# Kernel tuning notes

Measured on AMD Instinct MI355X. Metric: run time of the kernel, lower is better.

The kernel has to match this reference:

```python
import jax, jax.numpy as jnp
import numpy as np

DIM, HEADS, FFN, E = 1024, 16, 4096, 8
B, S = 2, 1024
EPS = 1e-5


def _ln(x, g, b):
    mu = jnp.mean(x, axis=-1, keepdims=True)
    var = jnp.mean((x - mu) ** 2, axis=-1, keepdims=True)
    return (x - mu) * jax.lax.rsqrt(var + EPS) * g + b


def setup_inputs() -> dict:
    key = jax.random.key(0)
    ks = jax.random.split(key, 20)
    sd = 0.02
    d, f = DIM, FFN
    return {
        "x": jax.random.normal(ks[0], (B, S, d), jnp.float32),
        "ln1_g": jnp.ones((d,), jnp.float32), "ln1_b": jnp.zeros((d,), jnp.float32),
        "Wqkv": jax.random.normal(ks[1], (d, 3 * d), jnp.float32) * sd,
        "bqkv": jnp.zeros((3 * d,), jnp.float32),
        "Wo": jax.random.normal(ks[2], (d, d), jnp.float32) * sd,
        "bo": jnp.zeros((d,), jnp.float32),
        "ln2_g": jnp.ones((d,), jnp.float32), "ln2_b": jnp.zeros((d,), jnp.float32),
        "gate_w": jax.random.normal(ks[3], (d, E), jnp.float32) * sd,
        "W1": jax.random.normal(ks[4], (E, d, f), jnp.float32) * sd,
        "b1": jnp.zeros((E, f), jnp.float32),
        "W2": jax.random.normal(ks[5], (E, f, d), jnp.float32) * sd,
        "b2": jnp.zeros((E, d), jnp.float32),
        "rW1": jax.random.normal(ks[6], (d, f), jnp.float32) * sd,
        "rb1": jnp.zeros((f,), jnp.float32),
        "rW2": jax.random.normal(ks[7], (f, d), jnp.float32) * sd,
        "rb2": jnp.zeros((d,), jnp.float32),
        "coef_w": jax.random.normal(ks[8], (d, 2), jnp.float32) * sd,
        "coef_b": jnp.zeros((2,), jnp.float32),
    }


def reference(x, ln1_g, ln1_b, Wqkv, bqkv, Wo, bo, ln2_g, ln2_b, gate_w,
              W1, b1, W2, b2, rW1, rb1, rW2, rb2, coef_w, coef_b):
    b, s, d = x.shape
    h, dh = HEADS, d // HEADS

    # --- attention block ---
    xn = _ln(x, ln1_g, ln1_b)
    qkv = xn @ Wqkv + bqkv                       # [b,s,3d]
    q, k, v = jnp.split(qkv, 3, axis=-1)
    q = q.reshape(b, s, h, dh)
    k = k.reshape(b, s, h, dh)
    v = v.reshape(b, s, h, dh)
    scores = jnp.einsum("bqhd,bkhd->bhqk", q, k) / jnp.sqrt(jnp.float32(dh))
    attn = jax.nn.softmax(scores, axis=-1)
    ctx = jnp.einsum("bhqk,bkhd->bqhd", attn, v).reshape(b, s, d)
    x = x + ctx @ Wo + bo

    # --- MoE FFN block (top-1 gating, DeepSpeed residual MoE) ---
    xn2 = _ln(x, ln2_g, ln2_b)
    xt = xn2.reshape(b * s, d)                   # [T,d] tokens
    probs = jax.nn.softmax(xt @ gate_w, axis=-1)  # [T,E]
    gate_val = jnp.max(probs, axis=-1, keepdims=True)   # top-1 prob
    expert_idx = jnp.argmax(probs, axis=-1)
    oh = jax.nn.one_hot(expert_idx, E, dtype=xt.dtype)  # [T,E] dispatch mask

    xe = jnp.einsum("te,td->etd", oh, xt)        # dispatch [E,T,d]
    he = jax.nn.gelu(jnp.einsum("etd,edf->etf", xe, W1) + b1[:, None, :], approximate=False)
    ye = jnp.einsum("etf,efd->etd", he, W2) + b2[:, None, :]
    moe_out = jnp.einsum("te,etd->td", oh, ye) * gate_val  # combine [T,d]

    # residual dense expert + learned mixing coefficient
    rm = jax.nn.gelu(xt @ rW1 + rb1, approximate=False) @ rW2 + rb2
    coef = jax.nn.softmax(xt @ coef_w + coef_b, axis=-1)  # [T,2]
    ff = moe_out * coef[:, 0:1] + rm * coef[:, 1:2]

    return x + ff.reshape(b, s, d)
```

## Files before the change

### kernel.cpp

```cpp
#include <hip/hip_runtime.h>
#include <math.h>

#define TOK 2048
#define NDIM 1024

typedef __attribute__((ext_vector_type(4))) float f32x4;
typedef __attribute__((ext_vector_type(8))) short s16x8;
typedef __attribute__((ext_vector_type(4))) short s16x4;

__device__ __forceinline__ short f2bf(float x) {
  unsigned int u = __builtin_bit_cast(unsigned int, x);
  unsigned int r = (u + 0x7fffu + ((u >> 16) & 1u)) >> 16;
  return (short)r;
}
__device__ __forceinline__ void gload_lds16(const void* g, void* l) {
  __builtin_amdgcn_global_load_lds((const __attribute__((address_space(1))) void*)g,
                                   (__attribute__((address_space(3))) void*)l, 16, 0, 0);
}

struct PackP { const float* src; short* dst; int K, N, nkt; };
__global__ __launch_bounds__(256)
void pack_k(PackP p)
{
  __shared__ float T[64 * 65];
  const int e = blockIdx.y;
  const int nkt = p.nkt;
  const int nt = blockIdx.x / nkt, kt = blockIdx.x % nkt;
  const float* src = p.src + (size_t)e * p.K * p.N + (size_t)(kt * 64) * p.N + nt * 64;
  const int t = threadIdx.x;
  #pragma unroll
  for (int i = 0; i < 16; ++i) {
    const int k = i * 4 + (t >> 6);
    T[k * 65 + (t & 63)] = src[(size_t)k * p.N + (t & 63)];
  }
  __syncthreads();
  short* dst = p.dst + ((size_t)e * gridDim.x + blockIdx.x) * 4096 + t * 16;
  s16x8 v[2];
  #pragma unroll
  for (int j2 = 0; j2 < 2; ++j2) {
    const int chunk = t * 2 + j2;
    const int col = chunk >> 3, od = chunk & 7, o = od ^ (col & 7);
    #pragma unroll
    for (int j = 0; j < 8; ++j) v[j2][j] = f2bf(T[(o * 8 + j) * 65 + col]);
  }
  *(s16x8*)dst = v[0];
  *(s16x8*)(dst + 8) = v[1];
}

__global__ __launch_bounds__(256)
void ln_k(const float* __restrict__ x, const float* __restrict__ g,
          const float* __restrict__ bb, short* __restrict__ out)
{
  const int row = blockIdx.x, tid = threadIdx.x;
  const f32x4 xv = *(const f32x4*)(x + (size_t)row * NDIM + tid * 4);
  float s = xv[0] + xv[1] + xv[2] + xv[3];
  float s2 = xv[0]*xv[0] + xv[1]*xv[1] + xv[2]*xv[2] + xv[3]*xv[3];
  #pragma unroll
  for (int m = 1; m < 64; m <<= 1) { s += __shfl_xor(s, m); s2 += __shfl_xor(s2, m); }
  __shared__ float red[8];
  const int w = tid >> 6, l = tid & 63;
  if (l == 0) { red[w] = s; red[4 + w] = s2; }
  __syncthreads();
  s = red[0] + red[1] + red[2] + red[3];
  s2 = red[4] + red[5] + red[6] + red[7];
  const float mean = s * (1.0f / NDIM);
  const float var = s2 * (1.0f / NDIM) - mean * mean;
  const float rstd = rsqrtf(var + 1e-5f);
  const f32x4 gv = *(const f32x4*)(g + tid * 4);
  const f32x4 bv = *(const f32x4*)(bb + tid * 4);
  s16x4 ov;
  #pragma unroll
  for (int j = 0; j < 4; ++j) ov[j] = f2bf((xv[j] - mean) * rstd * gv[j] + bv[j]);
  *(s16x4*)(out + (size_t)row * NDIM + tid * 4) = ov;
}

__global__ __launch_bounds__(256)
void gate_k(const float* __restrict__ x1, const float* __restrict__ g,
            const float* __restrict__ bb, const float* __restrict__ gw,
            const float* __restrict__ cw, const float* __restrict__ cb,
            int* __restrict__ counts, int* __restrict__ bucket,
            float* __restrict__ gs, float* __restrict__ c1o)
{
  const int tid = threadIdx.x, l = tid & 63, w = tid >> 6;
  const int t = blockIdx.x * 4 + w;
  f32x4 xv[4];
  #pragma unroll
  for (int it = 0; it < 4; ++it)
    xv[it] = *(const f32x4*)(x1 + (size_t)t * NDIM + it * 256 + l * 4);
  float s = 0.f, s2 = 0.f;
  #pragma unroll
  for (int it = 0; it < 4; ++it)
    #pragma unroll
    for (int j = 0; j < 4; ++j) { s += xv[it][j]; s2 += xv[it][j] * xv[it][j]; }
  #pragma unroll
  for (int m = 1; m < 64; m <<= 1) { s += __shfl_xor(s, m); s2 += __shfl_xor(s2, m); }
  const float mean = s * (1.0f / NDIM);
  const float rstd = rsqrtf(s2 * (1.0f / NDIM) - mean * mean + 1e-5f);
  float acc[10];
  #pragma unroll
  for (int j = 0; j < 10; ++j) acc[j] = 0.f;
  #pragma unroll
  for (int it = 0; it < 4; ++it) {
    #pragma unroll
    for (int j = 0; j < 4; ++j) {
      const int d0 = it * 256 + l * 4 + j;
      const float xn = (xv[it][j] - mean) * rstd * g[d0] + bb[d0];
      const f32x4 g0 = *(const f32x4*)(gw + (size_t)d0 * 8);
      const f32x4 g1 = *(const f32x4*)(gw + (size_t)d0 * 8 + 4);
      #pragma unroll
      for (int q = 0; q < 4; ++q) { acc[q] += xn * g0[q]; acc[4 + q] += xn * g1[q]; }
      acc[8] += xn * cw[d0 * 2]; acc[9] += xn * cw[d0 * 2 + 1];
    }
  }
  #pragma unroll
  for (int j = 0; j < 10; ++j)
    #pragma unroll
    for (int m = 1; m < 64; m <<= 1) acc[j] += __shfl_xor(acc[j], m);
  if (l == 0) {
    int best = 0; float mx = acc[0];
    #pragma unroll
    for (int e = 1; e < 8; ++e) if (acc[e] > mx) { mx = acc[e]; best = e; }
    float se = 0.f;
    #pragma unroll
    for (int e = 0; e < 8; ++e) se += __expf(acc[e] - mx);
    const float gate_val = 1.0f / se;
    const float l0 = acc[8] + cb[0], l1 = acc[9] + cb[1];
    const float cmx = fmaxf(l0, l1);
    const float e0 = __expf(l0 - cmx), e1 = __expf(l1 - cmx);
    const float inv = 1.0f / (e0 + e1);
    const int pos = atomicAdd(&counts[best], 1);
    bucket[best * TOK + pos] = t;
    gs[t] = gate_val * e0 * inv;
    c1o[t] = e1 * inv;
  }
}

struct GemmP {
  const short* A; const short* Bp; const float* bias;
  float* outf; short* outh;
  const float* resid; const float* aux; const float* sA; const float* sB;
  const int* bucket; const int* counts;
  int N, K, ktc;
};

template<int EPI, bool GATHER>
__global__ __launch_bounds__(256, 3)
void gemm_k(GemmP p)
{
  __shared__ short Al[2][8192];
  __shared__ short Bl[2][4096];
  const int tid = threadIdx.x;
  const int l = tid & 63, w = tid >> 6;
  const int wr = w >> 1, wc = w & 1;
  const int ntn = p.N >> 6, nkt = p.K >> 6;
  const int mt = blockIdx.x / ntn;
  const int nt = blockIdx.x % ntn;
  const int z = blockIdx.z;
  const bool first = (z == 0);
  const int K = p.K, N = p.N;

  int cnt = TOK;
  const short* Abase = p.A;
  const float* bias = p.bias;
  const int* bucket = nullptr;
  int e = 0;
  if (GATHER) {
    e = blockIdx.y;
    cnt = p.counts[e];
    if (mt * 128 >= cnt) return;
    bucket = p.bucket + e * TOK;
    bias = p.bias + (size_t)e * N;
  }
  const short* btile = p.Bp + ((size_t)(e * ntn + nt) * nkt) * 4096;

  const short* aptr[4];
  #pragma unroll
  for (int i = 0; i < 4; ++i) {
    const int rl = (i * 256 + tid) >> 3;
    int row;
    if (GATHER) {
      const int bidx = mt * 128 + rl;
      row = bucket[bidx < cnt ? bidx : mt * 128];
    } else row = mt * 128 + rl;
    aptr[i] = Abase + (size_t)row * K + ((tid & 7) ^ (rl & 7)) * 8;
  }

  const int kt0 = z * p.ktc, kt1 = kt0 + p.ktc;

  auto stage = [&](int kt, int buf) {
    const short* bsrc = btile + kt * 4096;
    #pragma unroll
    for (int j = 0; j < 2; ++j)
      gload_lds16(bsrc + (j * 256 + tid) * 8, (char*)Bl[buf] + (j * 256 + (tid & 192)) * 16);
    #pragma unroll
    for (int i = 0; i < 4; ++i)
      gload_lds16(aptr[i] + kt * 64, (char*)Al[buf] + (i * 256 + (tid & 192)) * 16);
  };

  f32x4 acc[4][2] = {};
  stage(kt0, 0);
  __syncthreads();
  for (int kt = kt0; kt < kt1; ++kt) {
    const int cur = (kt - kt0) & 1;
    if (kt + 1 < kt1) stage(kt + 1, cur ^ 1);
    #pragma unroll
    for (int ks = 0; ks < 2; ++ks) {
      const int octd = (ks * 4 + (l >> 4)) ^ (l & 7);
      s16x8 af[4], bfr[2];
      #pragma unroll
      for (int mf = 0; mf < 4; ++mf)
        af[mf] = *(const s16x8*)((char*)Al[cur] +
            (wr * 64 + mf * 16 + (l & 15)) * 128 + octd * 16);
      #pragma unroll
      for (int nf = 0; nf < 2; ++nf)
        bfr[nf] = *(const s16x8*)((char*)Bl[cur] +
            (wc * 32 + nf * 16 + (l & 15)) * 128 + octd * 16);
      #pragma unroll
      for (int mf = 0; mf < 4; ++mf)
        #pragma unroll
        for (int nf = 0; nf < 2; ++nf)
          acc[mf][nf] = __builtin_amdgcn_mfma_f32_16x16x32_bf16(af[mf], bfr[nf], acc[mf][nf], 0, 0, 0);
    }
    __syncthreads();
  }

  #pragma unroll
  for (int mf = 0; mf < 4; ++mf) {
    #pragma unroll
    for (int i = 0; i < 4; ++i) {
      const int rloc = wr * 64 + mf * 16 + (l >> 4) * 4 + i;
      int grow; bool valid = true;
      if (GATHER) {
        const int bidx = mt * 128 + rloc;
        valid = bidx < cnt;
        grow = valid ? bucket[bidx] : 0;
      } else grow = mt * 128 + rloc;
      float srow = 0.f;
      if (EPI == 3) srow = valid ? p.sA[grow] : 0.f;
      if (EPI == 4) srow = p.sB[grow];
      #pragma unroll
      for (int nf = 0; nf < 2; ++nf) {
        const int col = nt * 64 + wc * 32 + nf * 16 + (l & 15);
        const size_t off = (size_t)grow * N + col;
        const float bc = first ? bias[col] : 0.f;
        if (EPI == 0) {
          if (valid) p.outh[off] = f2bf(acc[mf][nf][i] + bc);
        } else if (EPI == 1) {
          const float v = acc[mf][nf][i] + bc;
          const float gv = 0.5f * v * (1.0f + erff(v * 0.70710678f));
          if (valid) p.outh[off] = f2bf(gv);
        } else if (EPI == 2) {
          atomicAdd(&p.outf[off], acc[mf][nf][i] + bc + (first ? p.resid[off] : 0.f));
        } else if (EPI == 3) {
          if (valid) atomicAdd(&p.outf[off], (acc[mf][nf][i] + bc) * srow);
        } else if (EPI == 4) {
          atomicAdd(&p.outf[off], (acc[mf][nf][i] + bc) * srow +
                    (first ? p.resid[off] + p.aux[off] : 0.f));
        }
      }
    }
  }
}

__global__ __launch_bounds__(256, 2)
void attn_k(const short* __restrict__ qkv, short* __restrict__ ctx)
{
  __shared__ short Klds[64 * 64];
  __shared__ short Vlds[64 * 64];
  __shared__ short Plds[4 * 16 * 64];
  const int tid = threadIdx.x, l = tid & 63, w = tid >> 6;
  const int qt = blockIdx.x;
  const int bh = blockIdx.y;
  const int b = bh >> 4, h = bh & 15;
  const size_t tbase = (size_t)b * 1024;

  const int sq = qt * 64 + w * 16 + (l & 15);
  s16x8 qf[2];
  #pragma unroll
  for (int ks = 0; ks < 2; ++ks)
    qf[ks] = *(const s16x8*)(qkv + (tbase + sq) * 3072 + h * 64 + ks * 32 + (l >> 4) * 8);

  f32x4 o[4] = {};
  float mrow[4], lrow[4];
  #pragma unroll
  for (int i = 0; i < 4; ++i) { mrow[i] = -1e30f; lrow[i] = 0.f; }

  for (int kt = 0; kt < 16; ++kt) {
    #pragma unroll
    for (int i = 0; i < 2; ++i) {
      const int s = i * 256 + tid;
      const int r = s >> 3, c = s & 7, csrc = c ^ (r & 7);
      const short* gsrc = qkv + (tbase + kt * 64 + r) * 3072 + 1024 + h * 64 + csrc * 8;
      gload_lds16(gsrc, (char*)Klds + (i * 256 + (tid & 192)) * 16);
    }
    #pragma unroll
    for (int i = 0; i < 2; ++i) {
      const int kv0 = (i * 4 + w) * 8;
      s16x8 vv;
      #pragma unroll
      for (int j = 0; j < 8; ++j)
        vv[j] = qkv[(tbase + kt * 64 + kv0 + j) * 3072 + 2048 + h * 64 + l];
      *(s16x8*)((char*)Vlds + ((l * 128 + kv0 * 2) ^ ((l & 7) << 4))) = vv;
    }
    __syncthreads();

    f32x4 sv[4];
    #pragma unroll
    for (int nf = 0; nf < 4; ++nf) {
      f32x4 a = {0.f, 0.f, 0.f, 0.f};
      const int kv = nf * 16 + (l & 15);
      #pragma unroll
      for (int ks = 0; ks < 2; ++ks) {
        const s16x8 kb = *(const s16x8*)((char*)Klds +
            ((kv * 128 + (ks * 32 + (l >> 4) * 8) * 2) ^ ((kv & 7) << 4)));
        a = __builtin_amdgcn_mfma_f32_16x16x32_bf16(qf[ks], kb, a, 0, 0, 0);
      }
      sv[nf] = a * 0.125f;
    }
    float sc[4], ps[4];
    #pragma unroll
    for (int i = 0; i < 4; ++i) {
      float m = fmaxf(fmaxf(sv[0][i], sv[1][i]), fmaxf(sv[2][i], sv[3][i]));
      #pragma unroll
      for (int msk = 1; msk < 16; msk <<= 1) m = fmaxf(m, __shfl_xor(m, msk));
      const float mn = fmaxf(mrow[i], m);
      sc[i] = __expf(mrow[i] - mn);
      mrow[i] = mn;
      ps[i] = 0.f;
    }
    #pragma unroll
    for (int nf = 0; nf < 4; ++nf)
      #pragma unroll
      for (int i = 0; i < 4; ++i) {
        const float pp = __expf(sv[nf][i] - mrow[i]);
        sv[nf][i] = pp;
        ps[i] += pp;
      }
    #pragma unroll
    for (int i = 0; i < 4; ++i) {
      #pragma unroll
      for (int msk = 1; msk < 16; msk <<= 1) ps[i] += __shfl_xor(ps[i], msk);
      lrow[i] = lrow[i] * sc[i] + ps[i];
    }
    #pragma unroll
    for (int nf = 0; nf < 4; ++nf)
      #pragma unroll
      for (int i = 0; i < 4; ++i) o[nf][i] *= sc[i];

    char* pw = (char*)Plds + w * 2048;
    #pragma unroll
    for (int nf = 0; nf < 4; ++nf)
      #pragma unroll
      for (int i = 0; i < 4; ++i) {
        const int q = (l >> 4) * 4 + i;
        *(short*)(pw + ((q * 128 + (nf * 16 + (l & 15)) * 2) ^ ((q & 7) << 4))) = f2bf(sv[nf][i]);
      }
    __syncthreads();
    #pragma unroll
    for (int ks = 0; ks < 2; ++ks) {
      const s16x8 pa = *(const s16x8*)(pw +
          (((l & 15) * 128 + (ks * 32 + (l >> 4) * 8) * 2) ^ ((l & 7) << 4)));
      #pragma unroll
      for (int nf = 0; nf < 4; ++nf) {
        const int dh = nf * 16 + (l & 15);
        const s16x8 vb = *(const s16x8*)((char*)Vlds +
            ((dh * 128 + (ks * 32 + (l >> 4) * 8) * 2) ^ ((dh & 7) << 4)));
        o[nf] = __builtin_amdgcn_mfma_f32_16x16x32_bf16(pa, vb, o[nf], 0, 0, 0);
      }
    }
    __syncthreads();
  }
  #pragma unroll
  for (int i = 0; i < 4; ++i) {
    const float inv = 1.0f / lrow[i];
    const size_t t = tbase + qt * 64 + w * 16 + (l >> 4) * 4 + i;
    #pragma unroll
    for (int nf = 0; nf < 4; ++nf)
      ctx[t * 1024 + h * 64 + nf * 16 + (l & 15)] = f2bf(o[nf][i] * inv);
  }
}

extern "C" void kernel_launch(void* const* d_in, const int* in_sizes, int n_in,
                              void* d_out, int out_size, void* d_ws, size_t ws_size,
                              hipStream_t stream)
{
  const float* x    = (const float*)d_in[0];
  const float* ln1g = (const float*)d_in[1];
  const float* ln1b = (const float*)d_in[2];
  const float* Wqkv = (const float*)d_in[3];
  const float* bqkv = (const float*)d_in[4];
  const float* Wo   = (const float*)d_in[5];
  const float* bo   = (const float*)d_in[6];
  const float* ln2g = (const float*)d_in[7];
  const float* ln2b = (const float*)d_in[8];
  const float* gw   = (const float*)d_in[9];
  const float* W1   = (const float*)d_in[10];
  const float* b1   = (const float*)d_in[11];
  const float* W2   = (const float*)d_in[12];
  const float* b2   = (const float*)d_in[13];
  const float* rW1  = (const float*)d_in[14];
  const float* rb1  = (const float*)d_in[15];
  const float* rW2  = (const float*)d_in[16];
  const float* rb2  = (const float*)d_in[17];
  const float* cw   = (const float*)d_in[18];
  const float* cb   = (const float*)d_in[19];
  float* out = (float*)d_out;

  char* ws = (char*)d_ws;
  const size_t MB = 1024 * 1024;
  short* xn1    = (short*)(ws + 0);
  short* qkv    = (short*)(ws + 4 * MB);
  short* he     = (short*)(ws + 4 * MB);
  short* ctx    = (short*)(ws + 16 * MB);
  float* x1     = (float*)(ws + 20 * MB);
  short* xn2    = (short*)(ws + 28 * MB);
  short* hr     = (short*)(ws + 32 * MB);
  float* moe    = (float*)(ws + 48 * MB);
  int*   counts = (int*)(ws + 56 * MB);
  int*   bucket = (int*)(ws + 56 * MB + 256);
  float* gs     = (float*)(ws + 56 * MB + 256 + 64 * 1024);
  float* c1     = (float*)(ws + 56 * MB + 256 + 64 * 1024 + 8192);
  short* Wqkvp  = (short*)(ws + 64 * MB);
  short* Wop    = (short*)(ws + 70 * MB);
  short* W1p    = (short*)(ws + 72 * MB);
  short* W2p    = (short*)(ws + 136 * MB);
  short* rW1p   = (short*)(ws + 200 * MB);
  short* rW2p   = (short*)(ws + 208 * MB);

  hipMemsetAsync(counts, 0, 8 * sizeof(int), stream);
  hipMemsetAsync(x1, 0, TOK * NDIM * sizeof(float), stream);
  hipMemsetAsync(moe, 0, TOK * NDIM * sizeof(float), stream);
  hipMemsetAsync(out, 0, TOK * NDIM * sizeof(float), stream);

  PackP pk;
  pk = PackP{Wqkv, Wqkvp, 1024, 3072, 16}; pack_k<<<dim3(48 * 16, 1), 256, 0, stream>>>(pk);
  pk = PackP{Wo,   Wop,   1024, 1024, 16}; pack_k<<<dim3(16 * 16, 1), 256, 0, stream>>>(pk);
  pk = PackP{W1,   W1p,   1024, 4096, 16}; pack_k<<<dim3(64 * 16, 8), 256, 0, stream>>>(pk);
  pk = PackP{W2,   W2p,   4096, 1024, 64}; pack_k<<<dim3(16 * 64, 8), 256, 0, stream>>>(pk);
  pk = PackP{rW1,  rW1p,  1024, 4096, 16}; pack_k<<<dim3(64 * 16, 1), 256, 0, stream>>>(pk);
  pk = PackP{rW2,  rW2p,  4096, 1024, 64}; pack_k<<<dim3(16 * 64, 1), 256, 0, stream>>>(pk);

  ln_k<<<TOK, 256, 0, stream>>>(x, ln1g, ln1b, xn1);

  GemmP p{};
  p.A = xn1; p.Bp = Wqkvp; p.bias = bqkv; p.outh = qkv; p.N = 3072; p.K = 1024; p.ktc = 16;
  gemm_k<0, false><<<dim3(16 * 48), 256, 0, stream>>>(p);

  attn_k<<<dim3(16, 32), 256, 0, stream>>>(qkv, ctx);

  p = GemmP{};
  p.A = ctx; p.Bp = Wop; p.bias = bo; p.outf = x1; p.resid = x; p.N = 1024; p.K = 1024; p.ktc = 8;
  gemm_k<2, false><<<dim3(16 * 16, 1, 2), 256, 0, stream>>>(p);

  ln_k<<<TOK, 256, 0, stream>>>(x1, ln2g, ln2b, xn2);
  gate_k<<<TOK / 4, 256, 0, stream>>>(x1, ln2g, ln2b, gw, cw, cb, counts, bucket, gs, c1);

  p = GemmP{};
  p.A = xn2; p.Bp = W1p; p.bias = b1; p.outh = he; p.N = 4096; p.K = 1024; p.ktc = 16;
  p.bucket = bucket; p.counts = counts;
  gemm_k<1, true><<<dim3(16 * 64, 8), 256, 0, stream>>>(p);

  p = GemmP{};
  p.A = he; p.Bp = W2p; p.bias = b2; p.outf = moe; p.sA = gs; p.N = 1024; p.K = 4096; p.ktc = 16;
  p.bucket = bucket; p.counts = counts;
  gemm_k<3, true><<<dim3(16 * 16, 8, 4), 256, 0, stream>>>(p);

  p = GemmP{};
  p.A = xn2; p.Bp = rW1p; p.bias = rb1; p.outh = hr; p.N = 4096; p.K = 1024; p.ktc = 16;
  gemm_k<1, false><<<dim3(16 * 64), 256, 0, stream>>>(p);

  p = GemmP{};
  p.A = hr; p.Bp = rW2p; p.bias = rb2; p.outf = out; p.resid = x1; p.aux = moe; p.sB = c1;
  p.N = 1024; p.K = 4096; p.ktc = 16;
  gemm_k<4, false><<<dim3(16 * 16, 1, 4), 256, 0, stream>>>(p);
}
```

Before: 511.3 us.

## Merge dense residual FFN into grouped MoE GEMMs and tighten GEMM pipeline sync

The residual dense FFN GEMMs become a ninth 'expert' slice of the grouped W1 and W2 launches. The second of these accumulates straight into the output, so the separate moe buffer, its memset and two launches go away. The GEMM main loop replaces __syncthreads with explicit vmcnt waits and raw s_barrier, so the next tile's loads can stay in flight while the current tile is computed. The weight pack kernel now reads float4 rows and handles four 64-column tiles per block, which cuts block count and makes the global reads coalesced. The risks are more atomic contention on the output and a hand-written vmcnt(6) that must match the number of issued loads exactly.

Result: faster. 488.2 us (-4.5%).

```diff
diff --git a/kernel.cpp b/kernel.cpp
--- a/kernel.cpp
+++ b/kernel.cpp
@@ -22,29 +22,37 @@
 __global__ __launch_bounds__(256)
 void pack_k(PackP p)
 {
-  __shared__ float T[64 * 65];
-  const int e = blockIdx.y;
+  __shared__ short T[64][264];
   const int nkt = p.nkt;
-  const int nt = blockIdx.x / nkt, kt = blockIdx.x % nkt;
-  const float* src = p.src + (size_t)e * p.K * p.N + (size_t)(kt * 64) * p.N + nt * 64;
+  const int cb = blockIdx.x / nkt, kt = blockIdx.x % nkt;
+  const int ntn = p.N >> 6;
+  const float* src = p.src + (size_t)blockIdx.y * p.K * p.N + (size_t)(kt * 64) * p.N + cb * 256;
   const int t = threadIdx.x;
   #pragma unroll
   for (int i = 0; i < 16; ++i) {
-    const int k = i * 4 + (t >> 6);
-    T[k * 65 + (t & 63)] = src[(size_t)k * p.N + (t & 63)];
+    const int r = i * 4 + (t >> 6);
+    const f32x4 v = *(const f32x4*)(src + (size_t)r * p.N + (t & 63) * 4);
+    short* d = &T[r][(t & 63) * 4];
+    d[0] = f2bf(v[0]); d[1] = f2bf(v[1]); d[2] = f2bf(v[2]); d[3] = f2bf(v[3]);
   }
   __syncthreads();
-  short* dst = p.dst + ((size_t)e * gridDim.x + blockIdx.x) * 4096 + t * 16;
-  s16x8 v[2];
-  #pragma unroll
-  for (int j2 = 0; j2 < 2; ++j2) {
-    const int chunk = t * 2 + j2;
-    const int col = chunk >> 3, od = chunk & 7, o = od ^ (col & 7);
-    #pragma unroll
-    for (int j = 0; j < 8; ++j) v[j2][j] = f2bf(T[(o * 8 + j) * 65 + col]);
-  }
-  *(s16x8*)dst = v[0];
-  *(s16x8*)(dst + 8) = v[1];
+  #pragma unroll
+  for (int j = 0; j < 4; ++j) {
+    short* dst = p.dst + ((size_t)(blockIdx.y * ntn + cb * 4 + j) * nkt + kt) * 4096 + t * 16;
+    s16x8 v0, v1;
+    #pragma unroll
+    for (int jj = 0; jj < 2; ++jj) {
+      const int chunk = t * 2 + jj;
+      const int col = chunk >> 3, od = chunk & 7, o = od ^ (col & 7);
+      #pragma unroll
+      for (int kk = 0; kk < 8; ++kk) {
+        const short vv = T[o * 8 + kk][j * 64 + col];
+        if (jj == 0) v0[kk] = vv; else v1[kk] = vv;
+      }
+    }
+    *(s16x8*)dst = v0;
+    *(s16x8*)(dst + 8) = v1;
+  }
 }
 
 __global__ __launch_bounds__(256)
@@ -136,14 +144,15 @@
 }
 
 struct GemmP {
-  const short* A; const short* Bp; const float* bias;
-  float* outf; short* outh;
-  const float* resid; const float* aux; const float* sA; const float* sB;
+  const short* A; const short* A2; const short* Bp; const short* Bp2;
+  const float* bias; const float* bias2;
+  short* outh; short* outh2; float* outf;
+  const float* resid; const float* gs; const float* c1;
   const int* bucket; const int* counts;
   int N, K, ktc;
 };
 
-template<int EPI, bool GATHER>
+template<int MODE>
 __global__ __launch_bounds__(256, 3)
 void gemm_k(GemmP p)
 {
@@ -159,26 +168,29 @@
   const bool first = (z == 0);
   const int K = p.K, N = p.N;
 
-  int cnt = TOK;
-  const short* Abase = p.A;
-  const float* bias = p.bias;
+  int e = 0, cnt = TOK;
   const int* bucket = nullptr;
-  int e = 0;
-  if (GATHER) {
+  if (MODE >= 2) {
     e = blockIdx.y;
-    cnt = p.counts[e];
-    if (mt * 128 >= cnt) return;
-    bucket = p.bucket + e * TOK;
-    bias = p.bias + (size_t)e * N;
-  }
-  const short* btile = p.Bp + ((size_t)(e * ntn + nt) * nkt) * 4096;
+    if (e < 8) {
+      cnt = p.counts[e];
+      if (mt * 128 >= cnt) return;
+      bucket = p.bucket + e * TOK;
+    }
+  }
+  const short* Abase = (MODE == 3 && e == 8) ? p.A2 : p.A;
+  const float* bias = (MODE >= 2) ? (e < 8 ? p.bias + (size_t)e * N : p.bias2) : p.bias;
+  const short* btile = (MODE >= 2)
+      ? (e < 8 ? p.Bp + ((size_t)(e * ntn + nt) * nkt) * 4096
+               : p.Bp2 + ((size_t)nt * nkt) * 4096)
+      : p.Bp + ((size_t)nt * nkt) * 4096;
 
   const short* aptr[4];
   #pragma unroll
   for (int i = 0; i < 4; ++i) {
     const int rl = (i * 256 + tid) >> 3;
     int row;
-    if (GATHER) {
+    if (bucket) {
       const int bidx = mt * 128 + rl;
       row = bucket[bidx < cnt ? bidx : mt * 128];
     } else row = mt * 128 + rl;
@@ -199,10 +211,15 @@
 
   f32x4 acc[4][2] = {};
   stage(kt0, 0);
-  __syncthreads();
   for (int kt = kt0; kt < kt1; ++kt) {
     const int cur = (kt - kt0) & 1;
-    if (kt + 1 < kt1) stage(kt + 1, cur ^ 1);
+    if (kt + 1 < kt1) {
+      stage(kt + 1, cur ^ 1);
+      asm volatile("s_waitcnt vmcnt(6)" ::: "memory");
+    } else {
+      asm volatile("s_waitcnt vmcnt(0)" ::: "memory");
+    }
+    __builtin_amdgcn_s_barrier();
     #pragma unroll
     for (int ks = 0; ks < 2; ++ks) {
       const int octd = (ks * 4 + (l >> 4)) ^ (l & 7);
@@ -221,41 +238,41 @@
         for (int nf = 0; nf < 2; ++nf)
           acc[mf][nf] = __builtin_amdgcn_mfma_f32_16x16x32_bf16(af[mf], bfr[nf], acc[mf][nf], 0, 0, 0);
     }
-    __syncthreads();
-  }
-
+    asm volatile("" ::: "memory");
+    __builtin_amdgcn_s_barrier();
+  }
+
+  short* oh = (MODE == 2) ? (e < 8 ? p.outh : p.outh2) : p.outh;
   #pragma unroll
   for (int mf = 0; mf < 4; ++mf) {
     #pragma unroll
     for (int i = 0; i < 4; ++i) {
       const int rloc = wr * 64 + mf * 16 + (l >> 4) * 4 + i;
       int grow; bool valid = true;
-      if (GATHER) {
+      if (bucket) {
         const int bidx = mt * 128 + rloc;
         valid = bidx < cnt;
         grow = valid ? bucket[bidx] : 0;
       } else grow = mt * 128 + rloc;
-      float srow = 0.f;
-      if (EPI == 3) srow = valid ? p.sA[grow] : 0.f;
-      if (EPI == 4) srow = p.sB[grow];
+      float srow = 1.f;
+      if (MODE == 3) srow = (e < 8) ? (valid ? p.gs[grow] : 0.f) : p.c1[grow];
       #pragma unroll
       for (int nf = 0; nf < 2; ++nf) {
         const int col = nt * 64 + wc * 32 + nf * 16 + (l & 15);
         const size_t off = (size_t)grow * N + col;
         const float bc = first ? bias[col] : 0.f;
-        if (EPI == 0) {
-          if (valid) p.outh[off] = f2bf(acc[mf][nf][i] + bc);
-        } else if (EPI == 1) {
+        if (MODE == 0) {
+          oh[off] = f2bf(acc[mf][nf][i] + bc);
+        } else if (MODE == 1) {
+          atomicAdd(&p.outf[off], acc[mf][nf][i] + bc + (first ? p.resid[off] : 0.f));
+        } else if (MODE == 2) {
           const float v = acc[mf][nf][i] + bc;
           const float gv = 0.5f * v * (1.0f + erff(v * 0.70710678f));
-          if (valid) p.outh[off] = f2bf(gv);
-        } else if (EPI == 2) {
-          atomicAdd(&p.outf[off], acc[mf][nf][i] + bc + (first ? p.resid[off] : 0.f));
-        } else if (EPI == 3) {
-          if (valid) atomicAdd(&p.outf[off], (acc[mf][nf][i] + bc) * srow);
-        } else if (EPI == 4) {
-          atomicAdd(&p.outf[off], (acc[mf][nf][i] + bc) * srow +
-                    (first ? p.resid[off] + p.aux[off] : 0.f));
+          if (valid) oh[off] = f2bf(gv);
+        } else if (MODE == 3) {
+          if (valid)
+            atomicAdd(&p.outf[off], (acc[mf][nf][i] + bc) * srow +
+                      ((e == 8 && first) ? p.resid[off] : 0.f));
         }
       }
     }
@@ -415,7 +432,6 @@
   float* x1     = (float*)(ws + 20 * MB);
   short* xn2    = (short*)(ws + 28 * MB);
   short* hr     = (short*)(ws + 32 * MB);
-  float* moe    = (float*)(ws + 48 * MB);
   int*   counts = (int*)(ws + 56 * MB);
   int*   bucket = (int*)(ws + 56 * MB + 256);
   float* gs     = (float*)(ws + 56 * MB + 256 + 64 * 1024);
@@ -429,48 +445,40 @@
 
   hipMemsetAsync(counts, 0, 8 * sizeof(int), stream);
   hipMemsetAsync(x1, 0, TOK * NDIM * sizeof(float), stream);
-  hipMemsetAsync(moe, 0, TOK * NDIM * sizeof(float), stream);
   hipMemsetAsync(out, 0, TOK * NDIM * sizeof(float), stream);
 
   PackP pk;
-  pk = PackP{Wqkv, Wqkvp, 1024, 3072, 16}; pack_k<<<dim3(48 * 16, 1), 256, 0, stream>>>(pk);
-  pk = PackP{Wo,   Wop,   1024, 1024, 16}; pack_k<<<dim3(16 * 16, 1), 256, 0, stream>>>(pk);
-  pk = PackP{W1,   W1p,   1024, 4096, 16}; pack_k<<<dim3(64 * 16, 8), 256, 0, stream>>>(pk);
-  pk = PackP{W2,   W2p,   4096, 1024, 64}; pack_k<<<dim3(16 * 64, 8), 256, 0, stream>>>(pk);
-  pk = PackP{rW1,  rW1p,  1024, 4096, 16}; pack_k<<<dim3(64 * 16, 1), 256, 0, stream>>>(pk);
-  pk = PackP{rW2,  rW2p,  4096, 1024, 64}; pack_k<<<dim3(16 * 64, 1), 256, 0, stream>>>(pk);
+  pk = PackP{Wqkv, Wqkvp, 1024, 3072, 16}; pack_k<<<dim3(12 * 16, 1), 256, 0, stream>>>(pk);
+  pk = PackP{Wo,   Wop,   1024, 1024, 16}; pack_k<<<dim3(4 * 16, 1), 256, 0, stream>>>(pk);
+  pk = PackP{W1,   W1p,   1024, 4096, 16}; pack_k<<<dim3(16 * 16, 8), 256, 0, stream>>>(pk);
+  pk = PackP{W2,   W2p,   4096, 1024, 64}; pack_k<<<dim3(4 * 64, 8), 256, 0, stream>>>(pk);
+  pk = PackP{rW1,  rW1p,  1024, 4096, 16}; pack_k<<<dim3(16 * 16, 1), 256, 0, stream>>>(pk);
+  pk = PackP{rW2,  rW2p,  4096, 1024, 64}; pack_k<<<dim3(4 * 64, 1), 256, 0, stream>>>(pk);
 
   ln_k<<<TOK, 256, 0, stream>>>(x, ln1g, ln1b, xn1);
 
   GemmP p{};
   p.A = xn1; p.Bp = Wqkvp; p.bias = bqkv; p.outh = qkv; p.N = 3072; p.K = 1024; p.ktc = 16;
-  gemm_k<0, false><<<dim3(16 * 48), 256, 0, stream>>>(p);
+  gemm_k<0><<<dim3(16 * 48), 256, 0, stream>>>(p);
 
   attn_k<<<dim3(16, 32), 256, 0, stream>>>(qkv, ctx);
 
   p = GemmP{};
   p.A = ctx; p.Bp = Wop; p.bias = bo; p.outf = x1; p.resid = x; p.N = 1024; p.K = 1024; p.ktc = 8;
-  gemm_k<2, false><<<dim3(16 * 16, 1, 2), 256, 0, stream>>>(p);
+  gemm_k<1><<<dim3(16 * 16, 1, 2), 256, 0, stream>>>(p);
 
   ln_k<<<TOK, 256, 0, stream>>>(x1, ln2g, ln2b, xn2);
   gate_k<<<TOK / 4, 256, 0, stream>>>(x1, ln2g, ln2b, gw, cw, cb, counts, bucket, gs, c1);
 
   p = GemmP{};
-  p.A = xn2; p.Bp = W1p; p.bias = b1; p.outh = he; p.N = 4096; p.K = 1024; p.ktc = 16;
+  p.A = xn2; p.Bp = W1p; p.Bp2 = rW1p; p.bias = b1; p.bias2 = rb1;
+  p.outh = he; p.outh2 = hr; p.N = 4096; p.K = 1024; p.ktc = 16;
   p.bucket = bucket; p.counts = counts;
-  gemm_k<1, true><<<dim3(16 * 64, 8), 256, 0, stream>>>(p);
+  gemm_k<2><<<dim3(16 * 64, 9), 256, 0, stream>>>(p);
 
   p = GemmP{};
-  p.A = he; p.Bp = W2p; p.bias = b2; p.outf = moe; p.sA = gs; p.N = 1024; p.K = 4096; p.ktc = 16;
+  p.A = he; p.A2 = hr; p.Bp = W2p; p.Bp2 = rW2p; p.bias = b2; p.bias2 = rb2;
+  p.outf = out; p.resid = x1; p.gs = gs; p.c1 = c1; p.N = 1024; p.K = 4096; p.ktc = 16;
   p.bucket = bucket; p.counts = counts;
-  gemm_k<3, true><<<dim3(16 * 16, 8, 4), 256, 0, stream>>>(p);
-
-  p = GemmP{};
-  p.A = xn2; p.Bp = rW1p; p.bias = rb1; p.outh = hr; p.N = 4096; p.K = 1024; p.ktc = 16;
-  gemm_k<1, false><<<dim3(16 * 64), 256, 0, stream>>>(p);
-
-  p = GemmP{};
-  p.A = hr; p.Bp = rW2p; p.bias = rb2; p.outf = out; p.resid = x1; p.aux = moe; p.sB = c1;
-  p.N = 1024; p.K = 4096; p.ktc = 16;
-  gemm_k<4, false><<<dim3(16 * 16, 1, 4), 256, 0, stream>>>(p);
-}
+  gemm_k<3><<<dim3(16 * 16, 9, 4), 256, 0, stream>>>(p);
+}
```
